# Performance work log

Hardware: AMD Instinct MI355X
Metric: run time of the kernel (lower is better)

Reference implementation:

```python
import jax, jax.numpy as jnp
import numpy as np

B, S, D, H = 4, 2048, 1024, 16
HD = D // H  # head dim = 64


def setup_inputs() -> dict:
    key = jax.random.key(0)
    ks = jax.random.split(key, 7)
    return {
        "hidden_states": jax.random.normal(ks[0], (B, S, D), jnp.float32),
        "attention_mask": jnp.zeros((B, 1, 1, S), jnp.float32),  # additive mask
        "Wq": jax.random.normal(ks[1], (D, D), jnp.float32) * 0.02,
        "bq": jax.random.normal(ks[2], (D,), jnp.float32) * 0.02,
        "Wk": jax.random.normal(ks[3], (D, D), jnp.float32) * 0.02,
        "bk": jax.random.normal(ks[4], (D,), jnp.float32) * 0.02,
        "Wv": jax.random.normal(ks[5], (D, D), jnp.float32) * 0.02,
        "bv": jax.random.normal(ks[6], (D,), jnp.float32) * 0.02,
    }


def _split_heads(x):
    # [B,S,D] -> [B,H,S,HD]
    b, s, _ = x.shape
    return x.reshape(b, s, H, HD).transpose(0, 2, 1, 3)


def reference(hidden_states, attention_mask, Wq, bq, Wk, bk, Wv, bv):
    # torch Linear: x @ W.T + b
    q = _split_heads(hidden_states @ Wq.T + bq)
    k = _split_heads(hidden_states @ Wk.T + bk)
    v = _split_heads(hidden_states @ Wv.T + bv)
    scale = 1.0 / np.sqrt(HD)
    # [B,H,S,S] attention scores (full materialization, as in source)
    scores = jnp.einsum("bhqd,bhkd->bhqk", q, k) * scale
    scores = scores + attention_mask
    probs = jax.nn.softmax(scores, axis=-1)
    ctx = jnp.einsum("bhqk,bhkd->bhqd", probs, v)
    # [B,H,S,HD] -> [B,S,D]
    ctx = ctx.transpose(0, 2, 1, 3).reshape(hidden_states.shape[0], -1, D)
    return ctx
```

## Files before the change

kernel.cpp:

```cpp
#include <hip/hip_runtime.h>


typedef __bf16 bf16;
typedef bf16  bf16x8 __attribute__((ext_vector_type(8)));
typedef bf16  bf16x4 __attribute__((ext_vector_type(4)));
typedef float f32x4  __attribute__((ext_vector_type(4)));
typedef float f32x16 __attribute__((ext_vector_type(16)));
typedef int   i32x2  __attribute__((ext_vector_type(2)));

#define MFMA16(A, B, C) __builtin_amdgcn_mfma_f32_16x16x32_bf16((A), (B), (C), 0, 0, 0)
#define MFMA32(A, B, C) __builtin_amdgcn_mfma_f32_32x32x16_bf16((A), (B), (C), 0, 0, 0)

constexpr int BB = 4, SS = 2048, DD = 1024, HH = 16, HD = 64;
constexpr float SCALE = 0.125f;
constexpr float LOG2E = 1.44269504088896f;
constexpr float SCALE_LOG2E = SCALE * LOG2E;

__device__ __forceinline__ float fast_exp2(float x) {
#if __has_builtin(__builtin_amdgcn_exp2f)
  return __builtin_amdgcn_exp2f(x);
#else
  return exp2f(x);
#endif
}

__device__ __forceinline__ bf16x8 cvt8(f32x4 a, f32x4 b) {
  bf16x8 r;
  r[0] = (bf16)a[0]; r[1] = (bf16)a[1]; r[2] = (bf16)a[2]; r[3] = (bf16)a[3];
  r[4] = (bf16)b[0]; r[5] = (bf16)b[1]; r[6] = (bf16)b[2]; r[7] = (bf16)b[3];
  return r;
}

__device__ __forceinline__ unsigned pack2(float lo, float hi) {
  union { bf16 h[2]; unsigned u; } r;
  r.h[0] = (bf16)lo; r.h[1] = (bf16)hi;
  return r.u;
}

__device__ __forceinline__ void swap32(unsigned &a, unsigned &b) {
#if __has_builtin(__builtin_amdgcn_permlane32_swap)
  i32x2 r = __builtin_amdgcn_permlane32_swap((int)a, (int)b, false, false);
  a = (unsigned)r[0]; b = (unsigned)r[1];
#else
  int hi = (int)((threadIdx.x >> 5) & 1);
  unsigned xa = (unsigned)__shfl_xor((int)a, 32);
  unsigned xb = (unsigned)__shfl_xor((int)b, 32);
  unsigned na = hi ? xb : a;
  unsigned nb = hi ? b  : xa;
  a = na; b = nb;
#endif
}

__device__ __forceinline__ void gload_lds16(const bf16* g, bf16* l) {
  __builtin_amdgcn_global_load_lds(
      (const __attribute__((address_space(1))) void*)g,
      (__attribute__((address_space(3))) void*)l, 16, 0, 0);
}

__global__ __launch_bounds__(256, 2) void qkv_gemm(
    const float* __restrict__ X,
    const float* __restrict__ Wq, const float* __restrict__ bq,
    const float* __restrict__ Wk, const float* __restrict__ bk,
    const float* __restrict__ Wv, const float* __restrict__ bv,
    bf16* __restrict__ Qo, bf16* __restrict__ Ko, bf16* __restrict__ Vt) {
  const int z = blockIdx.z;
  const float* W    = (z == 0) ? Wq : (z == 1) ? Wk : Wv;
  const float* bias = (z == 0) ? bq : (z == 1) ? bk : bv;

  __shared__ bf16 As[128 * 64];
  __shared__ bf16 Bs[128 * 64];

  const int tid  = threadIdx.x;
  const int lane = tid & 63;
  const int w    = tid >> 6;
  const int wr   = w >> 1, wc = w & 1;
  const int m0   = blockIdx.x * 128;
  const int n0   = blockIdx.y * 128;
  const int c    = lane & 15, g = lane >> 4;

  f32x4 acc[4][4];
#pragma unroll
  for (int i = 0; i < 4; ++i)
#pragma unroll
    for (int j = 0; j < 4; ++j) acc[i][j] = f32x4{0.f, 0.f, 0.f, 0.f};

  for (int k0 = 0; k0 < DD; k0 += 64) {
    __syncthreads();
#pragma unroll
    for (int it = 0; it < 4; ++it) {
      int idx = tid + it * 256;
      int row = idx >> 3, c8 = idx & 7;
      const f32x4* ga = (const f32x4*)(X + (size_t)(m0 + row) * DD + k0 + c8 * 8);
      f32x4 a0 = ga[0], a1 = ga[1];
      *(bf16x8*)(&As[row * 64 + ((c8 * 8) ^ ((row & 7) << 3))]) = cvt8(a0, a1);
      const f32x4* gb = (const f32x4*)(W + (size_t)(n0 + row) * DD + k0 + c8 * 8);
      f32x4 b0 = gb[0], b1 = gb[1];
      *(bf16x8*)(&Bs[row * 64 + ((c8 * 8) ^ ((row & 7) << 3))]) = cvt8(b0, b1);
    }
    __syncthreads();

#pragma unroll
    for (int kk = 0; kk < 64; kk += 32) {
      bf16x8 af[4], bfr[4];
#pragma unroll
      for (int m = 0; m < 4; ++m) {
        int row = wr * 64 + m * 16 + c;
        af[m] = *(const bf16x8*)(&As[row * 64 + ((kk + g * 8) ^ ((row & 7) << 3))]);
      }
#pragma unroll
      for (int n = 0; n < 4; ++n) {
        int row = wc * 64 + n * 16 + c;
        bfr[n] = *(const bf16x8*)(&Bs[row * 64 + ((kk + g * 8) ^ ((row & 7) << 3))]);
      }
#pragma unroll
      for (int m = 0; m < 4; ++m)
#pragma unroll
        for (int n = 0; n < 4; ++n)
          acc[m][n] = MFMA16(af[m], bfr[n], acc[m][n]);
    }
  }

#pragma unroll
  for (int n = 0; n < 4; ++n) {
    int colg = n0 + wc * 64 + n * 16 + c;
    float bv_ = bias[colg];
#pragma unroll
    for (int m = 0; m < 4; ++m) {
      int rowg = m0 + wr * 64 + m * 16 + g * 4;
      f32x4 a = acc[m][n];
      if (z < 2) {
        bf16* dst = (z == 0) ? Qo : Ko;
#pragma unroll
        for (int j = 0; j < 4; ++j)
          dst[(size_t)(rowg + j) * DD + colg] = (bf16)(a[j] + bv_);
      } else {
        int bi = rowg >> 11, s = rowg & 2047;
        int hh = colg >> 6, dd = colg & 63;
        bf16x4 pv;
#pragma unroll
        for (int j = 0; j < 4; ++j) pv[j] = (bf16)(a[j] + bv_);
        *(bf16x4*)(&Vt[(((size_t)bi * HH + hh) * HD + dd) * SS + s]) = pv;
      }
    }
  }
}

__global__ __launch_bounds__(256) void attn(
    const bf16* __restrict__ Q,
    const bf16* __restrict__ K,
    const bf16* __restrict__ Vt,
    const float* __restrict__ mask,
    float* __restrict__ out) {
  __shared__ bf16 Ks[2][64 * 64];
  __shared__ bf16 Vs[2][64 * 64];
  __shared__ float Ms[SS];

  const int bh = blockIdx.x;
  const int qb = blockIdx.y;
  const int b = bh >> 4, h = bh & 15;
  const int tid = threadIdx.x;
  const int lane = tid & 63;
  const int w = tid >> 6;
  const int l31 = lane & 31, hi = lane >> 5;
  const int hi4 = hi * 4, hi8 = hi * 8;
  const int qg = qb * 128 + w * 32 + l31;

  const bf16* qptr = Q + ((size_t)(b * SS + qg)) * DD + h * HD;
  bf16x8 qB[4];
#pragma unroll
  for (int ks = 0; ks < 4; ++ks)
    qB[ks] = *(const bf16x8*)(qptr + ks * 16 + hi8);

  const bf16* Kbase = K + ((size_t)b * SS) * DD + h * HD;
  const bf16* Vbase = Vt + ((size_t)bh * HD) * SS;

  const int lr = lane >> 3;
  const int lc = ((lane & 7) ^ lr) * 8;
  const int r0 = w * 16 + lr;
  const int dbase0 = (w * 16) * 64;
  const int dbase1 = (w * 16 + 8) * 64;

  f32x4 lacc = {0.f, 0.f, 0.f, 0.f};
  f32x16 acc[2] = {};

  {
    const float* mbase = mask + b * SS;
    f32x4 m0 = *(const f32x4*)(mbase + tid * 8);
    f32x4 m1 = *(const f32x4*)(mbase + tid * 8 + 4);
    *(f32x4*)(&Ms[tid * 8])     = m0 * LOG2E;
    *(f32x4*)(&Ms[tid * 8 + 4]) = m1 * LOG2E;
  }
  gload_lds16(Kbase + (size_t)r0 * DD + lc,       &Ks[0][dbase0]);
  gload_lds16(Kbase + (size_t)(r0 + 8) * DD + lc, &Ks[0][dbase1]);
  gload_lds16(Vbase + (size_t)r0 * SS + lc,       &Vs[0][dbase0]);
  gload_lds16(Vbase + (size_t)(r0 + 8) * SS + lc, &Vs[0][dbase1]);
  __syncthreads();

  for (int t2 = 0; t2 < 16; ++t2) {
#pragma unroll
    for (int half = 0; half < 2; ++half) {
      const int t = t2 * 2 + half;
      const int kv0 = t * 64;
      const bool last = (t == 31);

      if (!last) {
        const int sg = kv0 + 64;
        const int nb = half ^ 1;
        gload_lds16(Kbase + (size_t)(sg + r0) * DD + lc,       &Ks[nb][dbase0]);
        gload_lds16(Kbase + (size_t)(sg + r0 + 8) * DD + lc,   &Ks[nb][dbase1]);
        gload_lds16(Vbase + (size_t)r0 * SS + sg + lc,         &Vs[nb][dbase0]);
        gload_lds16(Vbase + (size_t)(r0 + 8) * SS + sg + lc,   &Vs[nb][dbase1]);
      }

      f32x16 st[2] = {};
      __builtin_amdgcn_s_setprio(1);
#pragma unroll
      for (int kvb = 0; kvb < 2; ++kvb) {
        const int krow = kvb * 32 + l31;
        const int kro = krow * 64, kr7 = krow & 7;
#pragma unroll
        for (int ks = 0; ks < 4; ++ks) {
          bf16x8 ka = *(const bf16x8*)(&Ks[half][kro + (((2 * ks + hi) ^ kr7) * 8)]);
          st[kvb] = MFMA32(ka, qB[ks], st[kvb]);
        }
      }
      __builtin_amdgcn_s_setprio(0);

      bf16x8 va[2][4];
#pragma unroll
      for (int db = 0; db < 2; ++db) {
        const int vrow = db * 32 + l31;
        const int vro = vrow * 64, vr7 = vrow & 7;
#pragma unroll
        for (int sl = 0; sl < 4; ++sl)
          va[db][sl] = *(const bf16x8*)(&Vs[half][vro + (((2 * sl + hi) ^ vr7) * 8)]);
      }

#pragma unroll
      for (int kvb = 0; kvb < 2; ++kvb) {
#pragma unroll
        for (int rg = 0; rg < 4; ++rg) {
          f32x4 mk = *(const f32x4*)(&Ms[kv0 + kvb * 32 + rg * 8 + hi4]);
#pragma unroll
          for (int j = 0; j < 4; ++j) {
            float e = fast_exp2(fmaf(st[kvb][rg * 4 + j], SCALE_LOG2E, mk[j]));
            st[kvb][rg * 4 + j] = e;
            lacc[j] += e;
          }
        }
      }

      __builtin_amdgcn_s_setprio(1);
#pragma unroll
      for (int kvb = 0; kvb < 2; ++kvb) {
#pragma unroll
        for (int s2 = 0; s2 < 2; ++s2) {
          unsigned L0 = pack2(st[kvb][8 * s2 + 0], st[kvb][8 * s2 + 1]);
          unsigned L1 = pack2(st[kvb][8 * s2 + 2], st[kvb][8 * s2 + 3]);
          unsigned H0 = pack2(st[kvb][8 * s2 + 4], st[kvb][8 * s2 + 5]);
          unsigned H1 = pack2(st[kvb][8 * s2 + 6], st[kvb][8 * s2 + 7]);
          swap32(L0, H0);
          swap32(L1, H1);
          union { unsigned u[4]; bf16x8 v; } pb;
          pb.u[0] = L0; pb.u[1] = L1; pb.u[2] = H0; pb.u[3] = H1;
          const int sl = kvb * 2 + s2;
          acc[0] = MFMA32(va[0][sl], pb.v, acc[0]);
          acc[1] = MFMA32(va[1][sl], pb.v, acc[1]);
        }
      }
      __builtin_amdgcn_s_setprio(0);

      __syncthreads();
    }
  }

  float ls = lacc[0] + lacc[1] + lacc[2] + lacc[3];
  ls += __shfl_xor(ls, 32);
  const float inv = 1.0f / ls;

  float* op = out + ((size_t)(b * SS + qg)) * DD + h * HD;
#pragma unroll
  for (int db = 0; db < 2; ++db)
#pragma unroll
    for (int rg = 0; rg < 4; ++rg) {
      f32x4 v;
#pragma unroll
      for (int j = 0; j < 4; ++j) v[j] = acc[db][rg * 4 + j] * inv;
      *(f32x4*)(op + db * 32 + rg * 8 + hi4) = v;
    }
}

extern "C" void kernel_launch(void* const* d_in, const int* in_sizes, int n_in,
                              void* d_out, int out_size, void* d_ws, size_t ws_size,
                              hipStream_t stream) {
  const float* X    = (const float*)d_in[0];
  const float* mask = (const float*)d_in[1];
  const float* Wq   = (const float*)d_in[2];
  const float* bq   = (const float*)d_in[3];
  const float* Wk   = (const float*)d_in[4];
  const float* bk   = (const float*)d_in[5];
  const float* Wv   = (const float*)d_in[6];
  const float* bv   = (const float*)d_in[7];

  bf16* Qw = (bf16*)d_ws;
  bf16* Kw = Qw + (size_t)BB * SS * DD;
  bf16* Vt = Kw + (size_t)BB * SS * DD;

  dim3 g1((BB * SS) / 128, DD / 128, 3);
  qkv_gemm<<<g1, 256, 0, stream>>>(X, Wq, bq, Wk, bk, Wv, bv, Qw, Kw, Vt);

  dim3 g2(BB * HH, SS / 128);
  attn<<<g2, 256, 0, stream>>>(Qw, Kw, Vt, mask, (float*)d_out);
}
```

Measured before the change: 200.8 us.

## Pre-convert inputs to bf16 and use direct-to-LDS loads in QKV GEMM

Adds a conversion kernel that casts X and the three weight matrices to bf16 once, staging them in the output buffer as scratch. The QKV GEMM then loads bf16 tiles straight into LDS with global_load_lds instead of loading fp32 and converting in registers, which halves global traffic per tile and removes per-tile conversion work. The attention kernel is also reworked: it uses a flat LDS buffer with precomputed offsets, seeds the score accumulators from the mask, and advances pointers incrementally. The mask is pre-multiplied by 8.0 so that the shared scale by SCALE*LOG2E yields mask*LOG2E, which keeps the math equivalent. The cost is an extra kernel launch and an extra read/write pass over the inputs.

```diff
diff --git a/kernel.cpp b/kernel.cpp
--- a/kernel.cpp
+++ b/kernel.cpp
@@ -12,6 +12,8 @@
 #define MFMA32(A, B, C) __builtin_amdgcn_mfma_f32_32x32x16_bf16((A), (B), (C), 0, 0, 0)
 
 constexpr int BB = 4, SS = 2048, DD = 1024, HH = 16, HD = 64;
+constexpr int NX = BB * SS * DD;
+constexpr int NW = DD * DD;
 constexpr float SCALE = 0.125f;
 constexpr float LOG2E = 1.44269504088896f;
 constexpr float SCALE_LOG2E = SCALE * LOG2E;
@@ -57,14 +59,28 @@
       (__attribute__((address_space(3))) void*)l, 16, 0, 0);
 }
 
+__global__ __launch_bounds__(256) void cvt_bf16(
+    const float* __restrict__ X,  const float* __restrict__ Wq,
+    const float* __restrict__ Wk, const float* __restrict__ Wv,
+    bf16* __restrict__ Xb, bf16* __restrict__ Wb) {
+  int i = (blockIdx.x * 256 + threadIdx.x) * 8;
+  const float* src; bf16* dst; int off;
+  if (i < NX)               { src = X;  dst = Xb;          off = i; }
+  else if (i < NX + NW)     { src = Wq; dst = Wb;          off = i - NX; }
+  else if (i < NX + 2 * NW) { src = Wk; dst = Wb + NW;     off = i - NX - NW; }
+  else                      { src = Wv; dst = Wb + 2 * NW; off = i - NX - 2 * NW; }
+  f32x4 a = *(const f32x4*)(src + off);
+  f32x4 b = *(const f32x4*)(src + off + 4);
+  *(bf16x8*)(dst + off) = cvt8(a, b);
+}
+
 __global__ __launch_bounds__(256, 2) void qkv_gemm(
-    const float* __restrict__ X,
-    const float* __restrict__ Wq, const float* __restrict__ bq,
-    const float* __restrict__ Wk, const float* __restrict__ bk,
-    const float* __restrict__ Wv, const float* __restrict__ bv,
+    const bf16* __restrict__ Xb, const bf16* __restrict__ Wb,
+    const float* __restrict__ bq, const float* __restrict__ bk,
+    const float* __restrict__ bv,
     bf16* __restrict__ Qo, bf16* __restrict__ Ko, bf16* __restrict__ Vt) {
   const int z = blockIdx.z;
-  const float* W    = (z == 0) ? Wq : (z == 1) ? Wk : Wv;
+  const bf16*  W    = Wb + (size_t)z * NW;
   const float* bias = (z == 0) ? bq : (z == 1) ? bk : bv;
 
   __shared__ bf16 As[128 * 64];
@@ -78,6 +94,13 @@
   const int n0   = blockIdx.y * 128;
   const int c    = lane & 15, g = lane >> 4;
 
+  const int lr  = lane >> 3;
+  const int lcs = ((lane & 7) ^ lr) * 8;
+  const bf16* aSrc = Xb + (size_t)(m0 + w * 32 + lr) * DD + lcs;
+  const bf16* bSrc = W  + (size_t)(n0 + w * 32 + lr) * DD + lcs;
+  bf16* aDst = &As[(w * 32) * 64];
+  bf16* bDst = &Bs[(w * 32) * 64];
+
   f32x4 acc[4][4];
 #pragma unroll
   for (int i = 0; i < 4; ++i)
@@ -87,15 +110,9 @@
   for (int k0 = 0; k0 < DD; k0 += 64) {
     __syncthreads();
 #pragma unroll
-    for (int it = 0; it < 4; ++it) {
-      int idx = tid + it * 256;
-      int row = idx >> 3, c8 = idx & 7;
-      const f32x4* ga = (const f32x4*)(X + (size_t)(m0 + row) * DD + k0 + c8 * 8);
-      f32x4 a0 = ga[0], a1 = ga[1];
-      *(bf16x8*)(&As[row * 64 + ((c8 * 8) ^ ((row & 7) << 3))]) = cvt8(a0, a1);
-      const f32x4* gb = (const f32x4*)(W + (size_t)(n0 + row) * DD + k0 + c8 * 8);
-      f32x4 b0 = gb[0], b1 = gb[1];
-      *(bf16x8*)(&Bs[row * 64 + ((c8 * 8) ^ ((row & 7) << 3))]) = cvt8(b0, b1);
+    for (int cc = 0; cc < 4; ++cc) {
+      gload_lds16(aSrc + (size_t)cc * 8 * DD + k0, aDst + cc * 512);
+      gload_lds16(bSrc + (size_t)cc * 8 * DD + k0, bDst + cc * 512);
     }
     __syncthreads();
 
@@ -105,12 +122,12 @@
 #pragma unroll
       for (int m = 0; m < 4; ++m) {
         int row = wr * 64 + m * 16 + c;
-        af[m] = *(const bf16x8*)(&As[row * 64 + ((kk + g * 8) ^ ((row & 7) << 3))]);
+        af[m] = *(const bf16x8*)(&As[row * 64 + (((kk >> 3) + g) ^ (row & 7)) * 8]);
       }
 #pragma unroll
       for (int n = 0; n < 4; ++n) {
         int row = wc * 64 + n * 16 + c;
-        bfr[n] = *(const bf16x8*)(&Bs[row * 64 + ((kk + g * 8) ^ ((row & 7) << 3))]);
+        bfr[n] = *(const bf16x8*)(&Bs[row * 64 + (((kk >> 3) + g) ^ (row & 7)) * 8]);
       }
 #pragma unroll
       for (int m = 0; m < 4; ++m)
@@ -151,9 +168,7 @@
     const bf16* __restrict__ Vt,
     const float* __restrict__ mask,
     float* __restrict__ out) {
-  __shared__ bf16 Ks[2][64 * 64];
-  __shared__ bf16 Vs[2][64 * 64];
-  __shared__ float Ms[SS];
+  __shared__ __align__(16) char smem[40960];
 
   const int bh = blockIdx.x;
   const int qb = blockIdx.y;
@@ -171,14 +186,20 @@
   for (int ks = 0; ks < 4; ++ks)
     qB[ks] = *(const bf16x8*)(qptr + ks * 16 + hi8);
 
-  const bf16* Kbase = K + ((size_t)b * SS) * DD + h * HD;
-  const bf16* Vbase = Vt + ((size_t)bh * HD) * SS;
-
-  const int lr = lane >> 3;
-  const int lc = ((lane & 7) ^ lr) * 8;
-  const int r0 = w * 16 + lr;
-  const int dbase0 = (w * 16) * 64;
-  const int dbase1 = (w * 16 + 8) * 64;
+  int off[4];
+#pragma unroll
+  for (int x = 0; x < 4; ++x)
+    off[x] = l31 * 128 + (((2 * x + hi) ^ (l31 & 7)) * 16);
+
+  const int lr  = lane >> 3;
+  const int lc  = ((lane & 7) ^ lr) * 8;
+  const int r0  = w * 16 + lr;
+  const bf16* kpA = K  + ((size_t)b * SS + r0) * DD + h * HD + lc;
+  const bf16* kpB = kpA + (size_t)8 * DD;
+  const bf16* vpA = Vt + ((size_t)bh * HD + r0) * SS + lc;
+  const bf16* vpB = vpA + (size_t)8 * SS;
+  bf16* kD0 = (bf16*)(smem + w * 2048);
+  bf16* vD0 = (bf16*)(smem + 16384 + w * 2048);
 
   f32x4 lacc = {0.f, 0.f, 0.f, 0.f};
   f32x16 acc[2] = {};
@@ -187,78 +208,78 @@
     const float* mbase = mask + b * SS;
     f32x4 m0 = *(const f32x4*)(mbase + tid * 8);
     f32x4 m1 = *(const f32x4*)(mbase + tid * 8 + 4);
-    *(f32x4*)(&Ms[tid * 8])     = m0 * LOG2E;
-    *(f32x4*)(&Ms[tid * 8 + 4]) = m1 * LOG2E;
+    *(f32x4*)(smem + 32768 + tid * 32)      = m0 * 8.0f;
+    *(f32x4*)(smem + 32768 + tid * 32 + 16) = m1 * 8.0f;
   }
-  gload_lds16(Kbase + (size_t)r0 * DD + lc,       &Ks[0][dbase0]);
-  gload_lds16(Kbase + (size_t)(r0 + 8) * DD + lc, &Ks[0][dbase1]);
-  gload_lds16(Vbase + (size_t)r0 * SS + lc,       &Vs[0][dbase0]);
-  gload_lds16(Vbase + (size_t)(r0 + 8) * SS + lc, &Vs[0][dbase1]);
+  gload_lds16(kpA, kD0);
+  gload_lds16(kpB, kD0 + 512);
+  gload_lds16(vpA, vD0);
+  gload_lds16(vpB, vD0 + 512);
+  kpA += (size_t)64 * DD; kpB += (size_t)64 * DD;
+  vpA += 64;              vpB += 64;
   __syncthreads();
 
   for (int t2 = 0; t2 < 16; ++t2) {
 #pragma unroll
     for (int half = 0; half < 2; ++half) {
       const int t = t2 * 2 + half;
-      const int kv0 = t * 64;
       const bool last = (t == 31);
 
       if (!last) {
-        const int sg = kv0 + 64;
-        const int nb = half ^ 1;
-        gload_lds16(Kbase + (size_t)(sg + r0) * DD + lc,       &Ks[nb][dbase0]);
-        gload_lds16(Kbase + (size_t)(sg + r0 + 8) * DD + lc,   &Ks[nb][dbase1]);
-        gload_lds16(Vbase + (size_t)r0 * SS + sg + lc,         &Vs[nb][dbase0]);
-        gload_lds16(Vbase + (size_t)(r0 + 8) * SS + sg + lc,   &Vs[nb][dbase1]);
-      }
-
-      f32x16 st[2] = {};
+        bf16* kD = (bf16*)(smem + (half ^ 1) * 8192 + w * 2048);
+        bf16* vD = (bf16*)(smem + 16384 + (half ^ 1) * 8192 + w * 2048);
+        gload_lds16(kpA, kD);
+        gload_lds16(kpB, kD + 512);
+        gload_lds16(vpA, vD);
+        gload_lds16(vpB, vD + 512);
+        kpA += (size_t)64 * DD; kpB += (size_t)64 * DD;
+        vpA += 64;              vpB += 64;
+      }
+
+      const char* mb = smem + (t * 256 + hi4 * 4);
+      union { f32x16 v; f32x4 q[4]; } st[2];
+#pragma unroll
+      for (int kvb = 0; kvb < 2; ++kvb)
+#pragma unroll
+        for (int rg = 0; rg < 4; ++rg)
+          st[kvb].q[rg] = *(const f32x4*)(mb + 32768 + kvb * 128 + rg * 32);
+
       __builtin_amdgcn_s_setprio(1);
 #pragma unroll
       for (int kvb = 0; kvb < 2; ++kvb) {
-        const int krow = kvb * 32 + l31;
-        const int kro = krow * 64, kr7 = krow & 7;
 #pragma unroll
         for (int ks = 0; ks < 4; ++ks) {
-          bf16x8 ka = *(const bf16x8*)(&Ks[half][kro + (((2 * ks + hi) ^ kr7) * 8)]);
-          st[kvb] = MFMA32(ka, qB[ks], st[kvb]);
+          bf16x8 ka = *(const bf16x8*)(smem + off[ks] + kvb * 4096 + half * 8192);
+          st[kvb].v = MFMA32(ka, qB[ks], st[kvb].v);
         }
       }
       __builtin_amdgcn_s_setprio(0);
 
       bf16x8 va[2][4];
 #pragma unroll
-      for (int db = 0; db < 2; ++db) {
-        const int vrow = db * 32 + l31;
-        const int vro = vrow * 64, vr7 = vrow & 7;
+      for (int db = 0; db < 2; ++db)
 #pragma unroll
         for (int sl = 0; sl < 4; ++sl)
-          va[db][sl] = *(const bf16x8*)(&Vs[half][vro + (((2 * sl + hi) ^ vr7) * 8)]);
-      }
-
+          va[db][sl] = *(const bf16x8*)(smem + 16384 + off[sl] + db * 4096 + half * 8192);
+
+#pragma unroll
+      for (int kvb = 0; kvb < 2; ++kvb)
+#pragma unroll
+        for (int r = 0; r < 16; ++r) {
+          float e = fast_exp2(st[kvb].v[r] * SCALE_LOG2E);
+          st[kvb].v[r] = e;
+          lacc[r & 3] += e;
+        }
+
+      __builtin_amdgcn_s_setprio(1);
 #pragma unroll
       for (int kvb = 0; kvb < 2; ++kvb) {
 #pragma unroll
-        for (int rg = 0; rg < 4; ++rg) {
-          f32x4 mk = *(const f32x4*)(&Ms[kv0 + kvb * 32 + rg * 8 + hi4]);
-#pragma unroll
-          for (int j = 0; j < 4; ++j) {
-            float e = fast_exp2(fmaf(st[kvb][rg * 4 + j], SCALE_LOG2E, mk[j]));
-            st[kvb][rg * 4 + j] = e;
-            lacc[j] += e;
-          }
-        }
-      }
-
-      __builtin_amdgcn_s_setprio(1);
-#pragma unroll
-      for (int kvb = 0; kvb < 2; ++kvb) {
-#pragma unroll
         for (int s2 = 0; s2 < 2; ++s2) {
-          unsigned L0 = pack2(st[kvb][8 * s2 + 0], st[kvb][8 * s2 + 1]);
-          unsigned L1 = pack2(st[kvb][8 * s2 + 2], st[kvb][8 * s2 + 3]);
-          unsigned H0 = pack2(st[kvb][8 * s2 + 4], st[kvb][8 * s2 + 5]);
-          unsigned H1 = pack2(st[kvb][8 * s2 + 6], st[kvb][8 * s2 + 7]);
+          unsigned L0 = pack2(st[kvb].v[8 * s2 + 0], st[kvb].v[8 * s2 + 1]);
+          unsigned L1 = pack2(st[kvb].v[8 * s2 + 2], st[kvb].v[8 * s2 + 3]);
+          unsigned H0 = pack2(st[kvb].v[8 * s2 + 4], st[kvb].v[8 * s2 + 5]);
+          unsigned H1 = pack2(st[kvb].v[8 * s2 + 6], st[kvb].v[8 * s2 + 7]);
           swap32(L0, H0);
           swap32(L1, H1);
           union { unsigned u[4]; bf16x8 v; } pb;
@@ -303,11 +324,15 @@
   const float* bv   = (const float*)d_in[7];
 
   bf16* Qw = (bf16*)d_ws;
-  bf16* Kw = Qw + (size_t)BB * SS * DD;
-  bf16* Vt = Kw + (size_t)BB * SS * DD;
+  bf16* Kw = Qw + (size_t)NX;
+  bf16* Vt = Kw + (size_t)NX;
+  bf16* Xb = (bf16*)d_out;
+  bf16* Wb = Xb + (size_t)NX;
+
+  cvt_bf16<<<(NX + 3 * NW) / 2048, 256, 0, stream>>>(X, Wq, Wk, Wv, Xb, Wb);
 
   dim3 g1((BB * SS) / 128, DD / 128, 3);
-  qkv_gemm<<<g1, 256, 0, stream>>>(X, Wq, bq, Wk, bk, Wv, bv, Qw, Kw, Vt);
+  qkv_gemm<<<g1, 256, 0, stream>>>(Xb, Wb, bq, bk, bv, Qw, Kw, Vt);
 
   dim3 g2(BB * HH, SS / 128);
   attn<<<g2, 256, 0, stream>>>(Qw, Kw, Vt, mask, (float*)d_out);
```

After: 166.6 us. -17.0%, faster.
